# Performance work log

Hardware: AMD Instinct MI355X
Metric: run time of the kernel (lower is better)

The kernel has to match this reference:

```python
import jax, jax.numpy as jnp
import numpy as np

B, T, D = 64, 2048, 512
H = 64           # hidden_size
K, S = 3, 3      # kernel_size, stride
PAD = (K - 1) // 2
BATCH_FACTOR = 0.5


def _ceil_div(a, b):
    return -(-a // b)


def _conv1d(x, w, b, stride, padding):
    # x: [B, C_in, T], w: [C_out, C_in, K] (torch Conv1d layout), b: [C_out]
    y = jax.lax.conv_general_dilated(
        x, w, window_strides=(stride,), padding=[(padding, padding)],
        dimension_numbers=("NCH", "OIH", "NCH"))
    return y + b[None, :, None]


def _score_estimator(x, seq_lens, w1, b1, w2, b2):
    # x: [B, T, D] -> scores [B, T''], seq lens [B]
    xc = jnp.transpose(x, (0, 2, 1))                     # [B, D, T]
    h = _conv1d(xc, w1, b1, S, PAD)                      # [B, 2H, T']
    h = h.reshape(h.shape[0], H, 2, h.shape[-1]).max(axis=2)  # maxout pairs -> [B, H, T']
    s = _conv1d(h, w2, b2, S, PAD)[:, 0, :]              # [B, T'']
    sl = _ceil_div(seq_lens - K + 1 + 2 * PAD, S)
    sl = _ceil_div(sl - K + 1 + 2 * PAD, S)
    return s, sl


def setup_inputs() -> dict:
    key = jax.random.key(0)
    ks = jax.random.split(key, 6)
    x = jax.random.normal(ks[0], (B, T, D), dtype=jnp.float32)
    seq_lens = jax.random.randint(ks[1], (B,), T // 2, T + 1)
    w1 = jax.random.normal(ks[2], (2 * H, D, K), dtype=jnp.float32) * (1.0 / np.sqrt(D * K))
    b1 = jax.random.normal(ks[3], (2 * H,), dtype=jnp.float32) * 0.01
    w2 = jax.random.normal(ks[4], (1, H, K), dtype=jnp.float32) * (1.0 / np.sqrt(H * K))
    b2 = jax.random.normal(ks[5], (1,), dtype=jnp.float32) * 0.01
    return {"x": x, "seq_lens": seq_lens, "w1": w1, "b1": b1, "w2": w2, "b2": b2}


def reference(x, seq_lens, w1, b1, w2, b2):
    scores, scores_sl = _score_estimator(x, seq_lens, w1, b1, w2, b2)  # [B, T''], [B]
    # mean over (padded) time, rescaled by T''/seq_len (torch true division -> float)
    est = scores.mean(axis=1) * (scores.shape[1] / scores_sl.astype(jnp.float32))  # [B]
    k = int(scores.shape[0] * BATCH_FACTOR)
    _, idx = jax.lax.top_k(est, k)
    # torch builds a boolean mask + masked_select, which preserves original batch order
    idx = jnp.sort(idx)
    sel_lens = seq_lens[idx]                              # [B']
    x_sel = x[idx]                                        # [B', T, D]
    # torch also truncates time to max(sel_lens); drops only padding frames.
    # Done eagerly here (data-dependent shape, so not inside jit).
    max_time = int(jnp.max(sel_lens))
    x_sel = x_sel[:, :max_time, :]
    return x_sel, sel_lens
```

## Files before the change

### kernel.cpp

```cpp
#include <hip/hip_runtime.h>

#define T_LEN 2048
#define D_DIM 512
#define B_SZ  64
#define T1_LEN 683
#define NSEL  32
#define KTOT  1536
#define BK    64
#define TILE_T1 96
#define NTILES 8
#define NITER (KTOT / BK)

typedef __attribute__((ext_vector_type(8))) short bf16x8;
typedef __attribute__((ext_vector_type(4))) float f32x4;

constexpr size_t OFF_WHI = 0;
constexpr size_t OFF_WLO = 393216;
constexpr size_t OFF_EST = 786432;
constexpr size_t OFF_SEL = 786944;

__device__ inline unsigned bf16_rne(float x) {
    unsigned u = __float_as_uint(x);
    return (u + 0x7FFFu + ((u >> 16) & 1u)) >> 16;
}

__device__ __forceinline__ void gload_lds16(const void* g, void* l) {
    __builtin_amdgcn_global_load_lds(
        (const __attribute__((address_space(1))) unsigned int*)g,
        (__attribute__((address_space(3))) unsigned int*)l,
        16, 0, 0);
}

__global__ __launch_bounds__(256) void pack_w1_split(const float* __restrict__ w1,
                                                     unsigned short* __restrict__ whi,
                                                     unsigned short* __restrict__ wlo,
                                                     float* __restrict__ est_raw) {
    if (blockIdx.x == 0 && threadIdx.x < 64) est_raw[threadIdx.x] = 0.f;
    int idx = blockIdx.x * 256 + threadIdx.x;
    int k0blk = idx >> 13;
    int rem   = idx & 8191;
    int row   = rem >> 6;
    int col   = rem & 63;
    int c8s   = col >> 3;
    int e     = col & 7;
    int c8    = c8s ^ (row & 7);
    int kap   = (k0blk << 6) + (c8 << 3) + e;
    int k = kap >> 9, d = kap & 511;
    float v = w1[row * 1536 + d * 3 + k];
    unsigned hb = bf16_rne(v);
    float hf = __uint_as_float(hb << 16);
    whi[idx] = (unsigned short)hb;
    wlo[idx] = (unsigned short)bf16_rne(v - hf);
}

__global__ __launch_bounds__(256, 2) void conv1_mfma(
        const float* __restrict__ x,
        const unsigned short* __restrict__ whi,
        const unsigned short* __restrict__ wlo,
        const float* __restrict__ b1,
        const float* __restrict__ w2,
        float* __restrict__ est_raw) {
    __shared__ __align__(16) unsigned short Ahi[128 * 64];
    __shared__ __align__(16) unsigned short Alo[128 * 64];
    __shared__ __align__(16) unsigned short Bhi[96 * 64];
    __shared__ __align__(16) unsigned short Blo[96 * 64];
    __shared__ float b1s[128];
    __shared__ float w2s[192];
    __shared__ float red[256];

    const int tid  = threadIdx.x;
    const int lane = tid & 63;
    const int w    = tid >> 6;
    const int b    = blockIdx.y;
    const int t1g0 = blockIdx.x * TILE_T1;

    if (tid < 128) b1s[tid] = b1[tid];
    if (tid < 192) w2s[tid] = w2[tid];

    const float* xb = x + (size_t)b * (T_LEN * (size_t)D_DIM);

    const int l15  = lane & 15;
    const int quad = lane >> 4;
    const int c0w  = (w >> 1) * 64;
    const int t0w  = (w & 1) * 48;

    int offA[4], swA[4];
    #pragma unroll
    for (int mi = 0; mi < 4; ++mi) { int r = c0w + mi * 16 + l15; offA[mi] = r * 64; swA[mi] = r & 7; }
    int offB[3], swB[3];
    #pragma unroll
    for (int ni = 0; ni < 3; ++ni) { int r = t0w + ni * 16 + l15; offB[ni] = r * 64; swB[ni] = r & 7; }

    int bdst[3], gb[3], bok[3];
    #pragma unroll
    for (int q = 0; q < 3; ++q) {
        int id = tid + 256 * q;
        int row = id >> 3, c8 = id & 7;
        int t1abs = t1g0 + row;
        bok[q]  = (t1abs < T1_LEN);
        gb[q]   = 1536 * t1abs + c8 * 8 - 512;
        bdst[q] = row * 64 + ((c8 ^ (row & 7)) << 3);
    }

    f32x4 acc[4][3];
    #pragma unroll
    for (int mi = 0; mi < 4; ++mi)
        #pragma unroll
        for (int ni = 0; ni < 3; ++ni) acc[mi][ni] = (f32x4){0.f, 0.f, 0.f, 0.f};

    for (int it = 0; it < NITER; ++it) {
        const int k0 = it * BK;

        float4 bv0 = make_float4(0.f,0.f,0.f,0.f), bv1 = bv0, bv2 = bv0,
               bv3 = bv0, bv4 = bv0, bv5 = bv0;
        {
            int g0 = gb[0] + k0, g1 = gb[1] + k0, g2 = gb[2] + k0;
            if (bok[0] && g0 >= 0) { bv0 = *(const float4*)(xb + g0); bv1 = *(const float4*)(xb + g0 + 4); }
            if (bok[1] && g1 >= 0) { bv2 = *(const float4*)(xb + g1); bv3 = *(const float4*)(xb + g1 + 4); }
            if (bok[2] && g2 >= 0) { bv4 = *(const float4*)(xb + g2); bv5 = *(const float4*)(xb + g2 + 4); }
        }

        {
            const unsigned short* sH = whi + it * 8192 + tid * 8;
            const unsigned short* sL = wlo + it * 8192 + tid * 8;
            unsigned short* dH = Ahi + tid * 8;
            unsigned short* dL = Alo + tid * 8;
            #pragma unroll
            for (int s = 0; s < 4; ++s) {
                gload_lds16(sH + s * 2048, dH + s * 2048);
                gload_lds16(sL + s * 2048, dL + s * 2048);
            }
        }

        #pragma unroll
        for (int q = 0; q < 3; ++q) {
            float4 va = (q == 0) ? bv0 : (q == 1) ? bv2 : bv4;
            float4 vb = (q == 0) ? bv1 : (q == 1) ? bv3 : bv5;
            unsigned f0 = __float_as_uint(va.x), f1 = __float_as_uint(va.y);
            unsigned f2 = __float_as_uint(va.z), f3 = __float_as_uint(va.w);
            unsigned f4 = __float_as_uint(vb.x), f5 = __float_as_uint(vb.y);
            unsigned f6 = __float_as_uint(vb.z), f7 = __float_as_uint(vb.w);
            unsigned hp0 = __builtin_amdgcn_perm(f1, f0, 0x07060302u);
            unsigned hp1 = __builtin_amdgcn_perm(f3, f2, 0x07060302u);
            unsigned hp2 = __builtin_amdgcn_perm(f5, f4, 0x07060302u);
            unsigned hp3 = __builtin_amdgcn_perm(f7, f6, 0x07060302u);
            float r0 = va.x - __uint_as_float(f0 & 0xFFFF0000u);
            float r1 = va.y - __uint_as_float(f1 & 0xFFFF0000u);
            float r2 = va.z - __uint_as_float(f2 & 0xFFFF0000u);
            float r3 = va.w - __uint_as_float(f3 & 0xFFFF0000u);
            float r4 = vb.x - __uint_as_float(f4 & 0xFFFF0000u);
            float r5 = vb.y - __uint_as_float(f5 & 0xFFFF0000u);
            float r6 = vb.z - __uint_as_float(f6 & 0xFFFF0000u);
            float r7 = vb.w - __uint_as_float(f7 & 0xFFFF0000u);
            unsigned lp0 = __builtin_amdgcn_perm(__float_as_uint(r1), __float_as_uint(r0), 0x07060302u);
            unsigned lp1 = __builtin_amdgcn_perm(__float_as_uint(r3), __float_as_uint(r2), 0x07060302u);
            unsigned lp2 = __builtin_amdgcn_perm(__float_as_uint(r5), __float_as_uint(r4), 0x07060302u);
            unsigned lp3 = __builtin_amdgcn_perm(__float_as_uint(r7), __float_as_uint(r6), 0x07060302u);
            *(int4*)(Bhi + bdst[q]) = make_int4(hp0, hp1, hp2, hp3);
            *(int4*)(Blo + bdst[q]) = make_int4(lp0, lp1, lp2, lp3);
        }
        __syncthreads();

        #pragma unroll
        for (int ks = 0; ks < 2; ++ks) {
            const int ch = ks * 4 + quad;
            bf16x8 ah[4], al[4], bh[3], bl[3];
            #pragma unroll
            for (int mi = 0; mi < 4; ++mi) {
                int o = offA[mi] + ((ch ^ swA[mi]) << 3);
                ah[mi] = *(const bf16x8*)(Ahi + o);
                al[mi] = *(const bf16x8*)(Alo + o);
            }
            #pragma unroll
            for (int ni = 0; ni < 3; ++ni) {
                int o = offB[ni] + ((ch ^ swB[ni]) << 3);
                bh[ni] = *(const bf16x8*)(Bhi + o);
                bl[ni] = *(const bf16x8*)(Blo + o);
            }
            #pragma unroll
            for (int mi = 0; mi < 4; ++mi)
                #pragma unroll
                for (int ni = 0; ni < 3; ++ni) {
                    acc[mi][ni] = __builtin_amdgcn_mfma_f32_16x16x32_bf16(ah[mi], bh[ni], acc[mi][ni], 0, 0, 0);
                    acc[mi][ni] = __builtin_amdgcn_mfma_f32_16x16x32_bf16(ah[mi], bl[ni], acc[mi][ni], 0, 0, 0);
                    acc[mi][ni] = __builtin_amdgcn_mfma_f32_16x16x32_bf16(al[mi], bh[ni], acc[mi][ni], 0, 0, 0);
                }
        }
        __syncthreads();
    }

    float contrib = 0.f;
    #pragma unroll
    for (int mi = 0; mi < 4; ++mi) {
        const int cbase = c0w + mi * 16 + (quad << 2);
        const float bb0 = b1s[cbase], bb1 = b1s[cbase + 1];
        const float bb2 = b1s[cbase + 2], bb3 = b1s[cbase + 3];
        const int j0 = cbase >> 1;
        #pragma unroll
        for (int ni = 0; ni < 3; ++ni) {
            const int t1 = t1g0 + t0w + ni * 16 + l15;
            if (t1 < T1_LEN) {
                float p0 = fmaxf(acc[mi][ni][0] + bb0, acc[mi][ni][1] + bb1);
                float p1 = fmaxf(acc[mi][ni][2] + bb2, acc[mi][ni][3] + bb3);
                int r = (t1 + 1) % 3;
                contrib += p0 * w2s[j0 * 3 + r] + p1 * w2s[(j0 + 1) * 3 + r];
            }
        }
    }
    red[tid] = contrib;
    __syncthreads();
    for (int off = 128; off > 0; off >>= 1) {
        if (tid < off) red[tid] += red[tid + off];
        __syncthreads();
    }
    if (tid == 0) atomicAdd(est_raw + b, red[0]);
}

__global__ void select_k(const float* __restrict__ est_raw,
                         const float* __restrict__ b2,
                         const int* __restrict__ seq_lens,
                         int* __restrict__ sel,
                         float* __restrict__ out_lens) {
    const int i = threadIdx.x;
    __shared__ float e[64];
    const int L  = seq_lens[i];
    const int sl = ((L + 2) / 3 + 2) / 3;
    const float ei = (est_raw[i] + 228.0f * b2[0]) / (float)sl;
    e[i] = ei;
    __syncthreads();
    int rank = 0;
    for (int j = 0; j < 64; ++j) {
        float ej = e[j];
        rank += (ej > ei) || (ej == ei && j < i);
    }
    const bool selq = rank < NSEL;
    const unsigned long long m = __ballot(selq);
    if (selq) {
        int pos = __popcll(m & ((1ull << i) - 1ull));
        sel[pos] = i;
        out_lens[pos] = (float)L;
    }
}

__global__ __launch_bounds__(256) void gather_rows(const float* __restrict__ x,
                                                   const int* __restrict__ sel,
                                                   float* __restrict__ out,
                                                   int n4row) {
    const int i = blockIdx.y;
    const int v = blockIdx.x * 256 + threadIdx.x;
    if (v < n4row) {
        const int src = sel[i];
        const float4* xs = (const float4*)(x + (size_t)src * T_LEN * D_DIM);
        float4* od = (float4*)(out + (size_t)i * ((size_t)n4row * 4));
        od[v] = xs[v];
    }
}

extern "C" void kernel_launch(void* const* d_in, const int* in_sizes, int n_in,
                              void* d_out, int out_size, void* d_ws, size_t ws_size,
                              hipStream_t stream) {
    const float* x        = (const float*)d_in[0];
    const int*   seq_lens = (const int*)  d_in[1];
    const float* w1       = (const float*)d_in[2];
    const float* b1       = (const float*)d_in[3];
    const float* w2       = (const float*)d_in[4];
    const float* b2       = (const float*)d_in[5];
    float* out = (float*)d_out;

    char* ws = (char*)d_ws;
    unsigned short* whi = (unsigned short*)(ws + OFF_WHI);
    unsigned short* wlo = (unsigned short*)(ws + OFF_WLO);
    float* est_raw = (float*)(ws + OFF_EST);
    int*   sel     = (int*)  (ws + OFF_SEL);

    const int max_time = (out_size - NSEL) / (NSEL * D_DIM);

    pack_w1_split<<<768, 256, 0, stream>>>(w1, whi, wlo, est_raw);
    conv1_mfma<<<dim3(NTILES, B_SZ), 256, 0, stream>>>(x, whi, wlo, b1, w2, est_raw);
    select_k<<<1, 64, 0, stream>>>(est_raw, b2, seq_lens, sel,
                                   out + (size_t)NSEL * max_time * D_DIM);
    const int n4row = max_time * (D_DIM / 4);
    gather_rows<<<dim3((n4row + 255) / 256, NSEL), 256, 0, stream>>>(x, sel, out, n4row);
}
```

Measured before the change: 444.1 us.

## Stage fp32 activations via direct global-to-LDS loads and split to bf16 at read

The x tile is now copied straight from global memory into LDS as fp32 with global_load_lds, using a zeroed workspace buffer as the source for padded or out-of-range rows. The bf16 hi/lo split moves from the staging step into the MFMA operand read path. This is meant to remove the register round-trip and VALU packing before the barrier so activation loads run asynchronously like the weight loads. In exchange the split is redone by every wave that reads a B fragment, LDS traffic for B doubles, and the new XOR swizzle on fp32 layout may cause bank conflicts.

```diff
diff --git a/kernel.cpp b/kernel.cpp
--- a/kernel.cpp
+++ b/kernel.cpp
@@ -18,6 +18,7 @@
 constexpr size_t OFF_WLO = 393216;
 constexpr size_t OFF_EST = 786432;
 constexpr size_t OFF_SEL = 786944;
+constexpr size_t OFF_ZERO = 787072;
 
 __device__ inline unsigned bf16_rne(float x) {
     unsigned u = __float_as_uint(x);
@@ -34,8 +35,10 @@
 __global__ __launch_bounds__(256) void pack_w1_split(const float* __restrict__ w1,
                                                      unsigned short* __restrict__ whi,
                                                      unsigned short* __restrict__ wlo,
-                                                     float* __restrict__ est_raw) {
+                                                     float* __restrict__ est_raw,
+                                                     float* __restrict__ zbuf) {
     if (blockIdx.x == 0 && threadIdx.x < 64) est_raw[threadIdx.x] = 0.f;
+    if (blockIdx.x == 0 && threadIdx.x >= 64 && threadIdx.x < 128) zbuf[threadIdx.x - 64] = 0.f;
     int idx = blockIdx.x * 256 + threadIdx.x;
     int k0blk = idx >> 13;
     int rem   = idx & 8191;
@@ -59,11 +62,11 @@
         const unsigned short* __restrict__ wlo,
         const float* __restrict__ b1,
         const float* __restrict__ w2,
-        float* __restrict__ est_raw) {
+        float* __restrict__ est_raw,
+        const float* __restrict__ zbuf) {
     __shared__ __align__(16) unsigned short Ahi[128 * 64];
     __shared__ __align__(16) unsigned short Alo[128 * 64];
-    __shared__ __align__(16) unsigned short Bhi[96 * 64];
-    __shared__ __align__(16) unsigned short Blo[96 * 64];
+    __shared__ __align__(16) float Bf[96 * 64];
     __shared__ float b1s[128];
     __shared__ float w2s[192];
     __shared__ float red[256];
@@ -87,19 +90,20 @@
     int offA[4], swA[4];
     #pragma unroll
     for (int mi = 0; mi < 4; ++mi) { int r = c0w + mi * 16 + l15; offA[mi] = r * 64; swA[mi] = r & 7; }
-    int offB[3], swB[3];
-    #pragma unroll
-    for (int ni = 0; ni < 3; ++ni) { int r = t0w + ni * 16 + l15; offB[ni] = r * 64; swB[ni] = r & 7; }
-
-    int bdst[3], gb[3], bok[3];
-    #pragma unroll
-    for (int q = 0; q < 3; ++q) {
-        int id = tid + 256 * q;
-        int row = id >> 3, c8 = id & 7;
+    int rBo[3], jB[3];
+    #pragma unroll
+    for (int ni = 0; ni < 3; ++ni) { int r = t0w + ni * 16 + l15; rBo[ni] = r * 64; jB[ni] = r & 15; }
+
+    int bbase[6], bthr[6];
+    float* bdst[6];
+    #pragma unroll
+    for (int i = 0; i < 6; ++i) {
+        int row   = w * 24 + i * 4 + (lane >> 4);
         int t1abs = t1g0 + row;
-        bok[q]  = (t1abs < T1_LEN);
-        gb[q]   = 1536 * t1abs + c8 * 8 - 512;
-        bdst[q] = row * 64 + ((c8 ^ (row & 7)) << 3);
+        int c     = (lane & 15) ^ (row & 15);
+        bbase[i]  = 1536 * t1abs + c * 4 - 512;
+        bthr[i]   = (t1abs < T1_LEN) ? (512 - c * 4 - 1536 * t1abs) : 0x7FFFFFFF;
+        bdst[i]   = Bf + (w * 1536 + i * 256 + lane * 4);
     }
 
     f32x4 acc[4][3];
@@ -111,15 +115,11 @@
     for (int it = 0; it < NITER; ++it) {
         const int k0 = it * BK;
 
-        float4 bv0 = make_float4(0.f,0.f,0.f,0.f), bv1 = bv0, bv2 = bv0,
-               bv3 = bv0, bv4 = bv0, bv5 = bv0;
-        {
-            int g0 = gb[0] + k0, g1 = gb[1] + k0, g2 = gb[2] + k0;
-            if (bok[0] && g0 >= 0) { bv0 = *(const float4*)(xb + g0); bv1 = *(const float4*)(xb + g0 + 4); }
-            if (bok[1] && g1 >= 0) { bv2 = *(const float4*)(xb + g1); bv3 = *(const float4*)(xb + g1 + 4); }
-            if (bok[2] && g2 >= 0) { bv4 = *(const float4*)(xb + g2); bv5 = *(const float4*)(xb + g2 + 4); }
-        }
-
+        #pragma unroll
+        for (int i = 0; i < 6; ++i) {
+            const float* s = (k0 >= bthr[i]) ? (xb + (bbase[i] + k0)) : zbuf;
+            gload_lds16(s, bdst[i]);
+        }
         {
             const unsigned short* sH = whi + it * 8192 + tid * 8;
             const unsigned short* sL = wlo + it * 8192 + tid * 8;
@@ -131,34 +131,6 @@
                 gload_lds16(sL + s * 2048, dL + s * 2048);
             }
         }
-
-        #pragma unroll
-        for (int q = 0; q < 3; ++q) {
-            float4 va = (q == 0) ? bv0 : (q == 1) ? bv2 : bv4;
-            float4 vb = (q == 0) ? bv1 : (q == 1) ? bv3 : bv5;
-            unsigned f0 = __float_as_uint(va.x), f1 = __float_as_uint(va.y);
-            unsigned f2 = __float_as_uint(va.z), f3 = __float_as_uint(va.w);
-            unsigned f4 = __float_as_uint(vb.x), f5 = __float_as_uint(vb.y);
-            unsigned f6 = __float_as_uint(vb.z), f7 = __float_as_uint(vb.w);
-            unsigned hp0 = __builtin_amdgcn_perm(f1, f0, 0x07060302u);
-            unsigned hp1 = __builtin_amdgcn_perm(f3, f2, 0x07060302u);
-            unsigned hp2 = __builtin_amdgcn_perm(f5, f4, 0x07060302u);
-            unsigned hp3 = __builtin_amdgcn_perm(f7, f6, 0x07060302u);
-            float r0 = va.x - __uint_as_float(f0 & 0xFFFF0000u);
-            float r1 = va.y - __uint_as_float(f1 & 0xFFFF0000u);
-            float r2 = va.z - __uint_as_float(f2 & 0xFFFF0000u);
-            float r3 = va.w - __uint_as_float(f3 & 0xFFFF0000u);
-            float r4 = vb.x - __uint_as_float(f4 & 0xFFFF0000u);
-            float r5 = vb.y - __uint_as_float(f5 & 0xFFFF0000u);
-            float r6 = vb.z - __uint_as_float(f6 & 0xFFFF0000u);
-            float r7 = vb.w - __uint_as_float(f7 & 0xFFFF0000u);
-            unsigned lp0 = __builtin_amdgcn_perm(__float_as_uint(r1), __float_as_uint(r0), 0x07060302u);
-            unsigned lp1 = __builtin_amdgcn_perm(__float_as_uint(r3), __float_as_uint(r2), 0x07060302u);
-            unsigned lp2 = __builtin_amdgcn_perm(__float_as_uint(r5), __float_as_uint(r4), 0x07060302u);
-            unsigned lp3 = __builtin_amdgcn_perm(__float_as_uint(r7), __float_as_uint(r6), 0x07060302u);
-            *(int4*)(Bhi + bdst[q]) = make_int4(hp0, hp1, hp2, hp3);
-            *(int4*)(Blo + bdst[q]) = make_int4(lp0, lp1, lp2, lp3);
-        }
         __syncthreads();
 
         #pragma unroll
@@ -173,9 +145,34 @@
             }
             #pragma unroll
             for (int ni = 0; ni < 3; ++ni) {
-                int o = offB[ni] + ((ch ^ swB[ni]) << 3);
-                bh[ni] = *(const bf16x8*)(Bhi + o);
-                bl[ni] = *(const bf16x8*)(Blo + o);
+                int p0 = ((2 * ch)     ^ jB[ni]) << 2;
+                int p1 = ((2 * ch + 1) ^ jB[ni]) << 2;
+                float4 va = *(const float4*)(Bf + rBo[ni] + p0);
+                float4 vb = *(const float4*)(Bf + rBo[ni] + p1);
+                unsigned f0 = __float_as_uint(va.x), f1 = __float_as_uint(va.y);
+                unsigned f2 = __float_as_uint(va.z), f3 = __float_as_uint(va.w);
+                unsigned f4 = __float_as_uint(vb.x), f5 = __float_as_uint(vb.y);
+                unsigned f6 = __float_as_uint(vb.z), f7 = __float_as_uint(vb.w);
+                unsigned hp0 = __builtin_amdgcn_perm(f1, f0, 0x07060302u);
+                unsigned hp1 = __builtin_amdgcn_perm(f3, f2, 0x07060302u);
+                unsigned hp2 = __builtin_amdgcn_perm(f5, f4, 0x07060302u);
+                unsigned hp3 = __builtin_amdgcn_perm(f7, f6, 0x07060302u);
+                float r0 = va.x - __uint_as_float(f0 & 0xFFFF0000u);
+                float r1 = va.y - __uint_as_float(f1 & 0xFFFF0000u);
+                float r2 = va.z - __uint_as_float(f2 & 0xFFFF0000u);
+                float r3 = va.w - __uint_as_float(f3 & 0xFFFF0000u);
+                float r4 = vb.x - __uint_as_float(f4 & 0xFFFF0000u);
+                float r5 = vb.y - __uint_as_float(f5 & 0xFFFF0000u);
+                float r6 = vb.z - __uint_as_float(f6 & 0xFFFF0000u);
+                float r7 = vb.w - __uint_as_float(f7 & 0xFFFF0000u);
+                unsigned lp0 = __builtin_amdgcn_perm(__float_as_uint(r1), __float_as_uint(r0), 0x07060302u);
+                unsigned lp1 = __builtin_amdgcn_perm(__float_as_uint(r3), __float_as_uint(r2), 0x07060302u);
+                unsigned lp2 = __builtin_amdgcn_perm(__float_as_uint(r5), __float_as_uint(r4), 0x07060302u);
+                unsigned lp3 = __builtin_amdgcn_perm(__float_as_uint(r7), __float_as_uint(r6), 0x07060302u);
+                int4 hv = make_int4(hp0, hp1, hp2, hp3);
+                int4 lv = make_int4(lp0, lp1, lp2, lp3);
+                bh[ni] = __builtin_bit_cast(bf16x8, hv);
+                bl[ni] = __builtin_bit_cast(bf16x8, lv);
             }
             #pragma unroll
             for (int mi = 0; mi < 4; ++mi)
@@ -272,11 +269,12 @@
     unsigned short* wlo = (unsigned short*)(ws + OFF_WLO);
     float* est_raw = (float*)(ws + OFF_EST);
     int*   sel     = (int*)  (ws + OFF_SEL);
+    float* zbuf    = (float*)(ws + OFF_ZERO);
 
     const int max_time = (out_size - NSEL) / (NSEL * D_DIM);
 
-    pack_w1_split<<<768, 256, 0, stream>>>(w1, whi, wlo, est_raw);
-    conv1_mfma<<<dim3(NTILES, B_SZ), 256, 0, stream>>>(x, whi, wlo, b1, w2, est_raw);
+    pack_w1_split<<<768, 256, 0, stream>>>(w1, whi, wlo, est_raw, zbuf);
+    conv1_mfma<<<dim3(NTILES, B_SZ), 256, 0, stream>>>(x, whi, wlo, b1, w2, est_raw, zbuf);
     select_k<<<1, 64, 0, stream>>>(est_raw, b2, seq_lens, sel,
                                    out + (size_t)NSEL * max_time * D_DIM);
     const int n4row = max_time * (D_DIM / 4);
```

Measured after the change: 448.3 us. About the same (+1.0%).
